# Performance work log

Measured on AMD Instinct MI355X. Metric: run time of the kernel, lower is better.

## Reference

```python
import jax, jax.numpy as jnp
import numpy as np

B, S, DIM, H = 4, 1024, 1024, 16
DH = DIM // H
ROPE_THETA = 10000.0


def setup_inputs() -> dict:
    key = jax.random.key(0)
    ks = jax.random.split(key, 9)
    sc = 1.0 / np.sqrt(DIM)
    return {
        "x": jax.random.normal(ks[0], (B, S, DIM), dtype=jnp.float32),
        "Wq": jax.random.normal(ks[1], (DIM, DIM), dtype=jnp.float32) * sc,
        "bq": jax.random.normal(ks[2], (DIM,), dtype=jnp.float32) * 0.02,
        "Wk": jax.random.normal(ks[3], (DIM, DIM), dtype=jnp.float32) * sc,
        "bk": jax.random.normal(ks[4], (DIM,), dtype=jnp.float32) * 0.02,
        "Wv": jax.random.normal(ks[5], (DIM, DIM), dtype=jnp.float32) * sc,
        "bv": jax.random.normal(ks[6], (DIM,), dtype=jnp.float32) * 0.02,
        "Wo": jax.random.normal(ks[7], (DIM, DIM), dtype=jnp.float32) * sc,
        "bo": jax.random.normal(ks[8], (DIM,), dtype=jnp.float32) * 0.02,
    }


def _rope(x):
    # x: (B, S, H, DH). Equinox RotaryPositionalEmbedding (GPT-NeoX half-split style):
    # out = x * tile(cos, 2) + rotate_half(x) * tile(sin, 2)
    seq, d = x.shape[1], x.shape[-1]
    half = d // 2
    freqs = 1.0 / (ROPE_THETA ** (jnp.arange(0, d, 2, dtype=jnp.float32)[:half] / d))  # (half,)
    ang = jnp.outer(jnp.arange(seq, dtype=jnp.float32), freqs)  # (S, half)
    cos = jnp.tile(jnp.cos(ang), (1, 2))[None, :, None, :]  # (1, S, 1, d)
    sin = jnp.tile(jnp.sin(ang), (1, 2))[None, :, None, :]
    x1, x2 = jnp.split(x, 2, axis=-1)
    rot = jnp.concatenate((-x2, x1), axis=-1)  # rotate_half
    return x * cos + rot * sin


def reference(x, Wq, bq, Wk, bk, Wv, bv, Wo, bo):
    # Projections (eqx.nn.Linear: y = W @ x + b, W is (out, in))
    q = (jnp.einsum("bsd,ed->bse", x, Wq) + bq).reshape(B, S, H, DH)
    k = (jnp.einsum("bsd,ed->bse", x, Wk) + bk).reshape(B, S, H, DH)
    v = (jnp.einsum("bsd,ed->bse", x, Wv) + bv).reshape(B, S, H, DH)
    # RoPE on query/key heads (process_heads)
    q = _rope(q)
    k = _rope(k)
    # Scaled dot-product attention, no mask, inference mode
    logits = jnp.einsum("bqhd,bkhd->bhqk", q, k) / jnp.sqrt(jnp.float32(DH))
    w = jax.nn.softmax(logits, axis=-1)
    o = jnp.einsum("bhqk,bkhd->bqhd", w, v).reshape(B, S, DIM)
    return jnp.einsum("bsd,ed->bse", o, Wo) + bo
```

## Files before the change

kernel.cpp:

```cpp
#include <hip/hip_runtime.h>
#include <math.h>

#define B_   4
#define S_   1024
#define DIM_ 1024
#define H_   16
#define DH_  64
#define M_   (B_ * S_)
#define K_   1024

typedef __attribute__((ext_vector_type(8))) short bf16x8;
typedef __attribute__((ext_vector_type(4))) float f32x4;
#define MFMA16(a, b, c) __builtin_amdgcn_mfma_f32_16x16x32_bf16((a), (b), (c), 0, 0, 0)

__device__ __forceinline__ ushort f2bf(float f) {
    union { float f; unsigned u; } v; v.f = f;
    unsigned r = v.u + 0x7FFF + ((v.u >> 16) & 1);
    return (ushort)(r >> 16);
}

__device__ __forceinline__ unsigned pk_bf(float a, float b) {
    union { float f; unsigned u; } x, y; x.f = a; y.f = b;
    return __builtin_amdgcn_perm(y.u + 0x8000u, x.u + 0x8000u, 0x07060302u);
}

__device__ __forceinline__ void gload16(const void* g, void* lds) {
    __builtin_amdgcn_global_load_lds(
        (const __attribute__((address_space(1))) unsigned int*)g,
        (__attribute__((address_space(3))) unsigned int*)lds, 16, 0, 0);
}

__global__ __launch_bounds__(256) void conv_kernel(
    const float* __restrict__ x,  const float* __restrict__ Wq,
    const float* __restrict__ Wk, const float* __restrict__ Wv,
    const float* __restrict__ Wo,
    ushort* __restrict__ Xb, ushort* __restrict__ Wb, ushort* __restrict__ Wob)
{
    const int idx = blockIdx.x * 256 + threadIdx.x;
    const float4* src;
    ushort* dst;
    if (idx < 1048576) {
        src = reinterpret_cast<const float4*>(x) + idx;
        dst = Xb + (size_t)idx * 4;
    } else {
        const int w = idx - 1048576;
        const int which = w >> 18;
        const int off = w & 262143;
        const float* s = (which == 0) ? Wq : (which == 1) ? Wk : (which == 2) ? Wv : Wo;
        src = reinterpret_cast<const float4*>(s) + off;
        dst = (which < 3) ? (Wb + (size_t)which * 1048576 + (size_t)off * 4)
                          : (Wob + (size_t)off * 4);
    }
    float4 v = *src;
    ushort4 o;
    o.x = f2bf(v.x); o.y = f2bf(v.y); o.z = f2bf(v.z); o.w = f2bf(v.w);
    *reinterpret_cast<ushort4*>(dst) = o;
}

__global__ __launch_bounds__(256) void rope_table_kernel(float* __restrict__ cosT,
                                                         float* __restrict__ sinT)
{
    const int idx = blockIdx.x * 256 + threadIdx.x;
    const int s = idx >> 5, j = idx & 31;
    const float freq = powf(10000.0f, -(float)j * (1.0f / 32.0f));
    float sn, cs;
    sincosf((float)s * freq, &sn, &cs);
    cosT[idx] = cs;
    sinT[idx] = sn;
}

__global__ __launch_bounds__(256) void qkv_mfma_kernel(
    const ushort* __restrict__ Xb, const ushort* __restrict__ Wb,
    const float* __restrict__ bq, const float* __restrict__ bk,
    const float* __restrict__ bv,
    const float* __restrict__ cosT, const float* __restrict__ sinT,
    ushort* __restrict__ Qh, ushort* __restrict__ Ksw, ushort* __restrict__ Vsw)
{
    __shared__ ushort As[128 * 32];
    __shared__ ushort Bs[128 * 32];

    const int tid  = threadIdx.x;
    const int wave = tid >> 6;
    const int lane = tid & 63;
    const int l15  = lane & 15;
    const int quad = lane >> 4;
    const int wr   = wave & 1;
    const int wc   = wave >> 1;
    const int m0   = blockIdx.y * 128;
    const int n0   = blockIdx.x * 128;
    const int lrow = lane >> 2;
    const int lcol = (lane & 3) * 8;

    const ushort* Ag = Xb + (size_t)m0 * K_;
    const ushort* Bg = Wb + (size_t)n0 * K_;

    f32x4 acc[4][4];
    #pragma unroll
    for (int i = 0; i < 4; i++)
        #pragma unroll
        for (int j = 0; j < 4; j++) acc[i][j] = (f32x4){0.f, 0.f, 0.f, 0.f};

    for (int k0 = 0; k0 < K_; k0 += 32) {
        __syncthreads();
        #pragma unroll
        for (int j = 0; j < 2; j++) {
            const int rb = (j * 4 + wave) * 16;
            gload16(Ag + (size_t)(rb + lrow) * K_ + k0 + lcol, As + rb * 32);
            gload16(Bg + (size_t)(rb + lrow) * K_ + k0 + lcol, Bs + rb * 32);
        }
        __syncthreads();

        bf16x8 af[4], bf[4];
        #pragma unroll
        for (int i = 0; i < 4; i++)
            af[i] = *reinterpret_cast<const bf16x8*>(As + (wr * 64 + i * 16 + l15) * 32 + quad * 8);
        #pragma unroll
        for (int i = 0; i < 4; i++)
            bf[i] = *reinterpret_cast<const bf16x8*>(Bs + (wc * 64 + i * 16 + l15) * 32 + quad * 8);
        #pragma unroll
        for (int i = 0; i < 4; i++)
            #pragma unroll
            for (int j = 0; j < 4; j++)
                acc[i][j] = MFMA16(af[i], bf[j], acc[i][j]);
    }

    const int zone = n0 >> 10;
    const int nl0  = n0 & 1023;
    const int n_base = nl0 + wc * 64 + l15;
    const int h = (nl0 + wc * 64) >> 6;
    const int r_m0 = m0 + wr * 64 + quad * 4;

    if (zone < 2) {
        const float* bias = zone ? bk : bq;
        const float qsc = zone ? 1.0f : 0.125f;
        float bias_l[4];
        #pragma unroll
        for (int ni = 0; ni < 4; ni++) bias_l[ni] = bias[n_base + ni * 16];
        #pragma unroll
        for (int mi = 0; mi < 4; mi++)
            #pragma unroll
            for (int r = 0; r < 4; r++) {
                const int m = r_m0 + mi * 16 + r;
                const int b = m >> 10, s = m & 1023;
                const float cs0 = cosT[s * 32 + l15],      sn0 = sinT[s * 32 + l15];
                const float cs1 = cosT[s * 32 + 16 + l15], sn1 = sinT[s * 32 + 16 + l15];
                ushort* qrow = Qh + ((size_t)(b * H_ + h) * S_ + s) * DH_;
                const size_t kbase = (size_t)(b * H_ + h) * 65536 +
                                     (size_t)(s >> 4) * 1024 + (s & 15) * 8;
                #pragma unroll
                for (int ni = 0; ni < 4; ni++) {
                    const float c = acc[mi][ni][r] + bias_l[ni];
                    const float p = acc[mi][ni ^ 2][r] + bias_l[ni ^ 2];
                    const float cs = (ni & 1) ? cs1 : cs0;
                    const float sn = (ni & 1) ? sn1 : sn0;
                    const float val = (ni & 2) ? fmaf(p, sn, c * cs) : fmaf(-p, sn, c * cs);
                    if (zone == 0) {
                        qrow[ni * 16 + l15] = f2bf(val * qsc);
                    } else {
                        const int dh = ni * 16 + l15;
                        Ksw[kbase + (dh >> 5) * 512 + ((dh >> 3) & 3) * 128 + (dh & 7)] = f2bf(val);
                    }
                }
            }
    } else {
        float bias_l[4];
        #pragma unroll
        for (int ni = 0; ni < 4; ni++) bias_l[ni] = bv[n_base + ni * 16];
        #pragma unroll
        for (int mi = 0; mi < 4; mi++)
            #pragma unroll
            for (int r = 0; r < 4; r++) {
                const int m = r_m0 + mi * 16 + r;
                const int b = m >> 10, s = m & 1023;
                const size_t vbase = (size_t)(b * H_ + h) * 65536 +
                                     (size_t)(s >> 5) * 2048 + ((s >> 3) & 3) * 128 + (s & 7);
                #pragma unroll
                for (int ni = 0; ni < 4; ni++)
                    Vsw[vbase + ni * 512 + l15 * 8] = f2bf(acc[mi][ni][r] + bias_l[ni]);
            }
    }
}

__global__ __launch_bounds__(256) void out_mfma_kernel(
    const ushort* __restrict__ Ob, const ushort* __restrict__ Wob,
    const float* __restrict__ bo, float* __restrict__ out)
{
    __shared__ ushort As[128 * 32];
    __shared__ ushort Bs[128 * 32];

    const int tid  = threadIdx.x;
    const int wave = tid >> 6;
    const int lane = tid & 63;
    const int l15  = lane & 15;
    const int quad = lane >> 4;
    const int wr   = wave & 1;
    const int wc   = wave >> 1;
    const int m0   = blockIdx.y * 128;
    const int n0   = blockIdx.x * 128;
    const int lrow = lane >> 2;
    const int lcol = (lane & 3) * 8;

    const ushort* Ag = Ob + (size_t)m0 * K_;
    const ushort* Bg = Wob + (size_t)n0 * K_;

    f32x4 acc[4][4];
    #pragma unroll
    for (int i = 0; i < 4; i++)
        #pragma unroll
        for (int j = 0; j < 4; j++) acc[i][j] = (f32x4){0.f, 0.f, 0.f, 0.f};

    for (int k0 = 0; k0 < K_; k0 += 32) {
        __syncthreads();
        #pragma unroll
        for (int j = 0; j < 2; j++) {
            const int rb = (j * 4 + wave) * 16;
            gload16(Ag + (size_t)(rb + lrow) * K_ + k0 + lcol, As + rb * 32);
            gload16(Bg + (size_t)(rb + lrow) * K_ + k0 + lcol, Bs + rb * 32);
        }
        __syncthreads();

        bf16x8 af[4], bf[4];
        #pragma unroll
        for (int i = 0; i < 4; i++)
            af[i] = *reinterpret_cast<const bf16x8*>(As + (wr * 64 + i * 16 + l15) * 32 + quad * 8);
        #pragma unroll
        for (int i = 0; i < 4; i++)
            bf[i] = *reinterpret_cast<const bf16x8*>(Bs + (wc * 64 + i * 16 + l15) * 32 + quad * 8);
        #pragma unroll
        for (int i = 0; i < 4; i++)
            #pragma unroll
            for (int j = 0; j < 4; j++)
                acc[i][j] = MFMA16(af[i], bf[j], acc[i][j]);
    }

    const int n_base = n0 + wc * 64 + l15;
    float bias_l[4];
    #pragma unroll
    for (int ni = 0; ni < 4; ni++) bias_l[ni] = bo[n_base + ni * 16];
    const int r_m0 = m0 + wr * 64 + quad * 4;
    #pragma unroll
    for (int mi = 0; mi < 4; mi++)
        #pragma unroll
        for (int r = 0; r < 4; r++) {
            const int m = r_m0 + mi * 16 + r;
            float* row = out + (size_t)m * DIM_;
            #pragma unroll
            for (int ni = 0; ni < 4; ni++)
                row[n_base + ni * 16] = acc[mi][ni][r] + bias_l[ni];
        }
}

#define LDPK 72

__global__ __launch_bounds__(256) void attn_mfma_kernel(
    const ushort* __restrict__ Qh, const ushort* __restrict__ Ksw,
    const ushort* __restrict__ Vsw, ushort* __restrict__ O)
{
    const int bh = blockIdx.x >> 4;
    const int q0 = (blockIdx.x & 15) * 64;

    __shared__ ushort Ps[4][16 * LDPK];

    const int tid  = threadIdx.x;
    const int wave = tid >> 6;
    const int lane = tid & 63;
    const int l15  = lane & 15;
    const int quad = lane >> 4;

    const ushort* qp = Qh + ((size_t)bh * S_ + q0 + wave * 16 + l15) * DH_;
    const bf16x8 qf0 = *reinterpret_cast<const bf16x8*>(qp + quad * 8);
    const bf16x8 qf1 = *reinterpret_cast<const bf16x8*>(qp + 32 + quad * 8);

    const ushort* Kb = Ksw + (size_t)bh * 65536 + lane * 8;
    const ushort* Vb = Vsw + (size_t)bh * 65536 + lane * 8;
    ushort* pw = &Ps[wave][0];

    f32x4 o_acc[4];
    #pragma unroll
    for (int c = 0; c < 4; c++) o_acc[c] = (f32x4){0.f, 0.f, 0.f, 0.f};
    float rs = 0.f;

    for (int t = 0; t < 16; t++) {
        const ushort* kt = Kb + t * 4096;
        const ushort* vt = Vb + t * 4096;

        f32x4 sc[4];
        #pragma unroll
        for (int c = 0; c < 4; c++) {
            bf16x8 k0 = *reinterpret_cast<const bf16x8*>(kt + c * 1024);
            bf16x8 k1 = *reinterpret_cast<const bf16x8*>(kt + c * 1024 + 512);
            f32x4 s = (f32x4){0.f, 0.f, 0.f, 0.f};
            s = MFMA16(k0, qf0, s);
            s = MFMA16(k1, qf1, s);
            sc[c] = s;
        }

        bf16x8 vf[2][4];
        #pragma unroll
        for (int j = 0; j < 2; j++)
            #pragma unroll
            for (int c = 0; c < 4; c++)
                vf[j][c] = *reinterpret_cast<const bf16x8*>(vt + j * 2048 + c * 512);

        #pragma unroll
        for (int c = 0; c < 4; c++) {
            const float p0v = __expf(sc[c][0]);
            const float p1v = __expf(sc[c][1]);
            const float p2v = __expf(sc[c][2]);
            const float p3v = __expf(sc[c][3]);
            rs += (p0v + p1v) + (p2v + p3v);
            uint2 pk;
            pk.x = pk_bf(p0v, p1v);
            pk.y = pk_bf(p2v, p3v);
            *reinterpret_cast<uint2*>(pw + l15 * LDPK + c * 16 + quad * 4) = pk;
        }

        const bf16x8 p0 = *reinterpret_cast<const bf16x8*>(pw + l15 * LDPK + quad * 8);
        const bf16x8 p1 = *reinterpret_cast<const bf16x8*>(pw + l15 * LDPK + 32 + quad * 8);
        #pragma unroll
        for (int c = 0; c < 4; c++) {
            o_acc[c] = MFMA16(vf[0][c], p0, o_acc[c]);
            o_acc[c] = MFMA16(vf[1][c], p1, o_acc[c]);
        }
    }

    rs += __shfl_xor(rs, 16, 64);
    rs += __shfl_xor(rs, 32, 64);
    const float inv = 1.0f / rs;

    const int b = bh >> 4, h = bh & 15;
    const int qrow = q0 + wave * 16 + l15;
    ushort* dst = O + ((size_t)(b * S_ + qrow)) * DIM_ + h * 64;
    #pragma unroll
    for (int c = 0; c < 4; c++) {
        uint2 pk;
        pk.x = pk_bf(o_acc[c][0] * inv, o_acc[c][1] * inv);
        pk.y = pk_bf(o_acc[c][2] * inv, o_acc[c][3] * inv);
        *reinterpret_cast<uint2*>(dst + c * 16 + quad * 4) = pk;
    }
}


extern "C" void kernel_launch(void* const* d_in, const int* in_sizes, int n_in,
                              void* d_out, int out_size, void* d_ws, size_t ws_size,
                              hipStream_t stream) {
    const float* x  = (const float*)d_in[0];
    const float* Wq = (const float*)d_in[1];
    const float* bq = (const float*)d_in[2];
    const float* Wk = (const float*)d_in[3];
    const float* bk = (const float*)d_in[4];
    const float* Wv = (const float*)d_in[5];
    const float* bv = (const float*)d_in[6];
    const float* Wo = (const float*)d_in[7];
    const float* bo = (const float*)d_in[8];
    float* out = (float*)d_out;

    const size_t n_elem = (size_t)B_ * S_ * DIM_;
    ushort* Xb  = (ushort*)d_ws;
    ushort* Wb  = Xb + n_elem;
    ushort* Wob = Wb + 3 * 1048576;
    ushort* Qh  = Wob + 1048576;
    ushort* Ksw = Qh + n_elem;
    ushort* Vsw = Ksw + n_elem;
    ushort* Ob  = Vsw + n_elem;
    float* cosT = (float*)(Ob + n_elem);
    float* sinT = cosT + S_ * 32;

    conv_kernel<<<dim3(8192), 256, 0, stream>>>(x, Wq, Wk, Wv, Wo, Xb, Wb, Wob);
    rope_table_kernel<<<dim3(128), 256, 0, stream>>>(cosT, sinT);

    qkv_mfma_kernel<<<dim3(3072 / 128, M_ / 128), 256, 0, stream>>>(
        Xb, Wb, bq, bk, bv, cosT, sinT, Qh, Ksw, Vsw);

    attn_mfma_kernel<<<dim3(B_ * H_ * (S_ / 64)), 256, 0, stream>>>(Qh, Ksw, Vsw, Ob);

    out_mfma_kernel<<<dim3(DIM_ / 128, M_ / 128), 256, 0, stream>>>(Ob, Wob, bo, out);
}
```

Measured before the change: 212.4 us.

## Retile QKV and output GEMMs to 64x128 tiles with K=64 swizzled LDS

Both projection GEMMs change from 128x128 tiles with K-step 32 to 64x128 tiles with K-step 64. Each wave now computes a 32x64 sub-tile. The LDS layout gains an XOR swizzle on 16-byte chunks to avoid bank conflicts on the fragment reads. This doubles the grid size, which improves occupancy and load balance across the many CUs, and halves the number of barrier-synchronised K iterations. The cost is less operand reuse per block, since A is reloaded more often across N tiles.

```diff
diff --git a/kernel.cpp b/kernel.cpp
--- a/kernel.cpp
+++ b/kernel.cpp
@@ -76,59 +76,66 @@
     const float* __restrict__ cosT, const float* __restrict__ sinT,
     ushort* __restrict__ Qh, ushort* __restrict__ Ksw, ushort* __restrict__ Vsw)
 {
-    __shared__ ushort As[128 * 32];
-    __shared__ ushort Bs[128 * 32];
+    __shared__ ushort As[64 * 64];
+    __shared__ ushort Bs[128 * 64];
 
     const int tid  = threadIdx.x;
     const int wave = tid >> 6;
     const int lane = tid & 63;
     const int l15  = lane & 15;
     const int quad = lane >> 4;
-    const int wr   = wave & 1;
-    const int wc   = wave >> 1;
-    const int m0   = blockIdx.y * 128;
+    const int m0   = blockIdx.y * 64;
     const int n0   = blockIdx.x * 128;
-    const int lrow = lane >> 2;
-    const int lcol = (lane & 3) * 8;
-
-    const ushort* Ag = Xb + (size_t)m0 * K_;
-    const ushort* Bg = Wb + (size_t)n0 * K_;
-
-    f32x4 acc[4][4];
-    #pragma unroll
-    for (int i = 0; i < 4; i++)
+
+    const int h8 = lane >> 3;
+    const int c8 = (lane & 7) ^ h8;
+    const ushort* Aga = Xb + (size_t)(m0 + h8) * K_ + c8 * 8;
+    const ushort* Bga = Wb + (size_t)(n0 + h8) * K_ + c8 * 8;
+    const int xr = l15 & 7;
+
+    f32x4 acc[2][4];
+    #pragma unroll
+    for (int i = 0; i < 2; i++)
         #pragma unroll
         for (int j = 0; j < 4; j++) acc[i][j] = (f32x4){0.f, 0.f, 0.f, 0.f};
 
-    for (int k0 = 0; k0 < K_; k0 += 32) {
+    for (int k0 = 0; k0 < K_; k0 += 64) {
         __syncthreads();
         #pragma unroll
-        for (int j = 0; j < 2; j++) {
-            const int rb = (j * 4 + wave) * 16;
-            gload16(Ag + (size_t)(rb + lrow) * K_ + k0 + lcol, As + rb * 32);
-            gload16(Bg + (size_t)(rb + lrow) * K_ + k0 + lcol, Bs + rb * 32);
-        }
+        for (int j = 0; j < 2; j++)
+            gload16(Aga + (size_t)(wave * 16 + j * 8) * K_ + k0,
+                    As + (wave * 2 + j) * 512 + lane * 8);
+        #pragma unroll
+        for (int j = 0; j < 4; j++)
+            gload16(Bga + (size_t)(wave * 32 + j * 8) * K_ + k0,
+                    Bs + (wave * 4 + j) * 512 + lane * 8);
         __syncthreads();
 
-        bf16x8 af[4], bf[4];
-        #pragma unroll
-        for (int i = 0; i < 4; i++)
-            af[i] = *reinterpret_cast<const bf16x8*>(As + (wr * 64 + i * 16 + l15) * 32 + quad * 8);
-        #pragma unroll
-        for (int i = 0; i < 4; i++)
-            bf[i] = *reinterpret_cast<const bf16x8*>(Bs + (wc * 64 + i * 16 + l15) * 32 + quad * 8);
-        #pragma unroll
-        for (int i = 0; i < 4; i++)
-            #pragma unroll
-            for (int j = 0; j < 4; j++)
-                acc[i][j] = MFMA16(af[i], bf[j], acc[i][j]);
+        #pragma unroll
+        for (int s = 0; s < 2; s++) {
+            const int kc = ((s * 4 + quad) ^ xr) * 8;
+            bf16x8 af[2], bf[4];
+            #pragma unroll
+            for (int mi = 0; mi < 2; mi++)
+                af[mi] = *reinterpret_cast<const bf16x8*>(
+                    As + ((wave & 1) * 32 + mi * 16 + l15) * 64 + kc);
+            #pragma unroll
+            for (int nj = 0; nj < 4; nj++)
+                bf[nj] = *reinterpret_cast<const bf16x8*>(
+                    Bs + ((wave >> 1) * 64 + nj * 16 + l15) * 64 + kc);
+            #pragma unroll
+            for (int mi = 0; mi < 2; mi++)
+                #pragma unroll
+                for (int nj = 0; nj < 4; nj++)
+                    acc[mi][nj] = MFMA16(af[mi], bf[nj], acc[mi][nj]);
+        }
     }
 
     const int zone = n0 >> 10;
     const int nl0  = n0 & 1023;
-    const int n_base = nl0 + wc * 64 + l15;
-    const int h = (nl0 + wc * 64) >> 6;
-    const int r_m0 = m0 + wr * 64 + quad * 4;
+    const int n_base = nl0 + (wave >> 1) * 64 + l15;
+    const int h = (nl0 + (wave >> 1) * 64) >> 6;
+    const int r_m0 = m0 + (wave & 1) * 32 + quad * 4;
 
     if (zone < 2) {
         const float* bias = zone ? bk : bq;
@@ -137,7 +144,7 @@
         #pragma unroll
         for (int ni = 0; ni < 4; ni++) bias_l[ni] = bias[n_base + ni * 16];
         #pragma unroll
-        for (int mi = 0; mi < 4; mi++)
+        for (int mi = 0; mi < 2; mi++)
             #pragma unroll
             for (int r = 0; r < 4; r++) {
                 const int m = r_m0 + mi * 16 + r;
@@ -167,7 +174,7 @@
         #pragma unroll
         for (int ni = 0; ni < 4; ni++) bias_l[ni] = bv[n_base + ni * 16];
         #pragma unroll
-        for (int mi = 0; mi < 4; mi++)
+        for (int mi = 0; mi < 2; mi++)
             #pragma unroll
             for (int r = 0; r < 4; r++) {
                 const int m = r_m0 + mi * 16 + r;
@@ -185,61 +192,68 @@
     const ushort* __restrict__ Ob, const ushort* __restrict__ Wob,
     const float* __restrict__ bo, float* __restrict__ out)
 {
-    __shared__ ushort As[128 * 32];
-    __shared__ ushort Bs[128 * 32];
+    __shared__ ushort As[64 * 64];
+    __shared__ ushort Bs[128 * 64];
 
     const int tid  = threadIdx.x;
     const int wave = tid >> 6;
     const int lane = tid & 63;
     const int l15  = lane & 15;
     const int quad = lane >> 4;
-    const int wr   = wave & 1;
-    const int wc   = wave >> 1;
-    const int m0   = blockIdx.y * 128;
+    const int m0   = blockIdx.y * 64;
     const int n0   = blockIdx.x * 128;
-    const int lrow = lane >> 2;
-    const int lcol = (lane & 3) * 8;
-
-    const ushort* Ag = Ob + (size_t)m0 * K_;
-    const ushort* Bg = Wob + (size_t)n0 * K_;
-
-    f32x4 acc[4][4];
-    #pragma unroll
-    for (int i = 0; i < 4; i++)
+
+    const int h8 = lane >> 3;
+    const int c8 = (lane & 7) ^ h8;
+    const ushort* Aga = Ob + (size_t)(m0 + h8) * K_ + c8 * 8;
+    const ushort* Bga = Wob + (size_t)(n0 + h8) * K_ + c8 * 8;
+    const int xr = l15 & 7;
+
+    f32x4 acc[2][4];
+    #pragma unroll
+    for (int i = 0; i < 2; i++)
         #pragma unroll
         for (int j = 0; j < 4; j++) acc[i][j] = (f32x4){0.f, 0.f, 0.f, 0.f};
 
-    for (int k0 = 0; k0 < K_; k0 += 32) {
+    for (int k0 = 0; k0 < K_; k0 += 64) {
         __syncthreads();
         #pragma unroll
-        for (int j = 0; j < 2; j++) {
-            const int rb = (j * 4 + wave) * 16;
-            gload16(Ag + (size_t)(rb + lrow) * K_ + k0 + lcol, As + rb * 32);
-            gload16(Bg + (size_t)(rb + lrow) * K_ + k0 + lcol, Bs + rb * 32);
-        }
+        for (int j = 0; j < 2; j++)
+            gload16(Aga + (size_t)(wave * 16 + j * 8) * K_ + k0,
+                    As + (wave * 2 + j) * 512 + lane * 8);
+        #pragma unroll
+        for (int j = 0; j < 4; j++)
+            gload16(Bga + (size_t)(wave * 32 + j * 8) * K_ + k0,
+                    Bs + (wave * 4 + j) * 512 + lane * 8);
         __syncthreads();
 
-        bf16x8 af[4], bf[4];
-        #pragma unroll
-        for (int i = 0; i < 4; i++)
-            af[i] = *reinterpret_cast<const bf16x8*>(As + (wr * 64 + i * 16 + l15) * 32 + quad * 8);
-        #pragma unroll
-        for (int i = 0; i < 4; i++)
-            bf[i] = *reinterpret_cast<const bf16x8*>(Bs + (wc * 64 + i * 16 + l15) * 32 + quad * 8);
-        #pragma unroll
-        for (int i = 0; i < 4; i++)
-            #pragma unroll
-            for (int j = 0; j < 4; j++)
-                acc[i][j] = MFMA16(af[i], bf[j], acc[i][j]);
-    }
-
-    const int n_base = n0 + wc * 64 + l15;
+        #pragma unroll
+        for (int s = 0; s < 2; s++) {
+            const int kc = ((s * 4 + quad) ^ xr) * 8;
+            bf16x8 af[2], bf[4];
+            #pragma unroll
+            for (int mi = 0; mi < 2; mi++)
+                af[mi] = *reinterpret_cast<const bf16x8*>(
+                    As + ((wave & 1) * 32 + mi * 16 + l15) * 64 + kc);
+            #pragma unroll
+            for (int nj = 0; nj < 4; nj++)
+                bf[nj] = *reinterpret_cast<const bf16x8*>(
+                    Bs + ((wave >> 1) * 64 + nj * 16 + l15) * 64 + kc);
+            #pragma unroll
+            for (int mi = 0; mi < 2; mi++)
+                #pragma unroll
+                for (int nj = 0; nj < 4; nj++)
+                    acc[mi][nj] = MFMA16(af[mi], bf[nj], acc[mi][nj]);
+        }
+    }
+
+    const int n_base = n0 + (wave >> 1) * 64 + l15;
     float bias_l[4];
     #pragma unroll
     for (int ni = 0; ni < 4; ni++) bias_l[ni] = bo[n_base + ni * 16];
-    const int r_m0 = m0 + wr * 64 + quad * 4;
-    #pragma unroll
-    for (int mi = 0; mi < 4; mi++)
+    const int r_m0 = m0 + (wave & 1) * 32 + quad * 4;
+    #pragma unroll
+    for (int mi = 0; mi < 2; mi++)
         #pragma unroll
         for (int r = 0; r < 4; r++) {
             const int m = r_m0 + mi * 16 + r;
@@ -369,10 +383,10 @@
     conv_kernel<<<dim3(8192), 256, 0, stream>>>(x, Wq, Wk, Wv, Wo, Xb, Wb, Wob);
     rope_table_kernel<<<dim3(128), 256, 0, stream>>>(cosT, sinT);
 
-    qkv_mfma_kernel<<<dim3(3072 / 128, M_ / 128), 256, 0, stream>>>(
+    qkv_mfma_kernel<<<dim3(3072 / 128, M_ / 64), 256, 0, stream>>>(
         Xb, Wb, bq, bk, bv, cosT, sinT, Qh, Ksw, Vsw);
 
     attn_mfma_kernel<<<dim3(B_ * H_ * (S_ / 64)), 256, 0, stream>>>(Qh, Ksw, Vsw, Ob);
 
-    out_mfma_kernel<<<dim3(DIM_ / 128, M_ / 128), 256, 0, stream>>>(Ob, Wob, bo, out);
-}
+    out_mfma_kernel<<<dim3(DIM_ / 128, M_ / 64), 256, 0, stream>>>(Ob, Wob, bo, out);
+}
```

New measurement: 187.7 us. 1.13x faster.
